# Kernel tuning notes

Hardware: AMD Instinct MI355X
Metric: run time of the kernel (lower is better)

## Reference

```python
import jax, jax.numpy as jnp
import numpy as np

N = 50000   # nodes
E = 800000  # edges
D = 64      # hidden_channels (= in_channels)
L = 3       # num_layers
G = 512     # graphs in batch
S = 32      # s_channels
BN_EPS = 1e-5


def setup_inputs() -> dict:
    key = jax.random.key(0)
    ks = jax.random.split(key, 10)
    x = jax.random.normal(ks[0], (N, D), dtype=jnp.float32)
    edge_index = jax.random.randint(ks[1], (2, E), 0, N)
    batch = jnp.sort(jax.random.randint(ks[2], (N,), 0, G))
    mapping = jax.random.randint(ks[3], (G,), 0, N)
    edge_weight = jax.random.uniform(ks[4], (E,), dtype=jnp.float32)
    pooling_mask = jnp.ones((N,), dtype=jnp.float32)
    # per-layer GIN MLP params (stacked over layers)
    W1 = 0.05 * jax.random.normal(ks[5], (L, D, D), dtype=jnp.float32)
    b1 = jnp.zeros((L, D), jnp.float32)
    gamma = jnp.ones((L, D), jnp.float32)
    beta = jnp.zeros((L, D), jnp.float32)
    bn_mean = jnp.zeros((L, D), jnp.float32)
    bn_var = jnp.ones((L, D), jnp.float32)
    W2 = 0.05 * jax.random.normal(ks[6], (L, D, D), dtype=jnp.float32)
    b2 = jnp.zeros((L, D), jnp.float32)
    eps = jnp.zeros((L,), jnp.float32)  # train_eps=True, init 0
    lin_w = 0.05 * jax.random.normal(ks[7], (2 * D * L, S), dtype=jnp.float32)
    lin_b = jnp.zeros((S,), jnp.float32)
    return dict(x=x, edge_weight=edge_weight, pooling_mask=pooling_mask,
                W1=W1, b1=b1, gamma=gamma, beta=beta, bn_mean=bn_mean,
                bn_var=bn_var, W2=W2, b2=b2, eps=eps, lin_w=lin_w,
                lin_b=lin_b, edge_index=edge_index, batch=batch,
                mapping=mapping)


def _sgin_forward(x, edge_weight, pooling_mask, W1, b1, gamma, beta,
                  bn_mean, bn_var, W2, b2, eps, lin_w, lin_b,
                  edge_index, batch, mapping):
    src, dst = edge_index[0], edge_index[1]
    h = x  # dropout is identity in eval mode
    pooled = []
    for i in range(L):
        # GIN aggregation: sum_j w_ij * h_j  at target nodes
        msg = h[src] * edge_weight[:, None]            # [E, D]
        agg = jax.ops.segment_sum(msg, dst, num_segments=N)
        z = (1.0 + eps[i]) * h + agg                   # [N, D]
        # MLP: Linear -> BN(eval) -> ReLU -> Linear -> ReLU
        z = z @ W1[i] + b1[i]
        z = gamma[i] * (z - bn_mean[i]) * jax.lax.rsqrt(bn_var[i] + BN_EPS) + beta[i]
        z = jax.nn.relu(z)
        h = jax.nn.relu(z @ W2[i] + b2[i])
        # per-layer pooling: masked global add pool || center-node gather
        emb_add = jax.ops.segment_sum(h * pooling_mask[:, None], batch,
                                      num_segments=G)  # [G, D]
        emb_center = h[mapping]                          # [G, D]
        pooled.append(jnp.concatenate([emb_add, emb_center], axis=-1))
    hcat = jnp.concatenate(pooled, axis=1)               # [G, 2*D*L]
    return hcat @ lin_w + lin_b                          # [G, S]


def reference(x, edge_weight, pooling_mask, W1, b1, gamma, beta, bn_mean,
              bn_var, W2, b2, eps, lin_w, lin_b, edge_index, batch, mapping):
    return _sgin_forward(x, edge_weight, pooling_mask, W1, b1, gamma, beta,
                         bn_mean, bn_var, W2, b2, eps, lin_w, lin_b,
                         edge_index, batch, mapping)
```

## Files before the change

### kernel.cpp

```cpp
#include <hip/hip_runtime.h>
#include <hip/hip_fp16.h>

#define DD 64
#define HC 384
#define SS 32
#define BINW 256
#define BSH 8
#define CAP 8192
#define CHUNK 4096

__global__ __launch_bounds__(256) void prep_kernel(
    const float* __restrict__ x, __half* __restrict__ hh0,
    int* __restrict__ bin_cur, float* __restrict__ hcat,
    int nbins, int hcat4, int total)
{
  int gid = blockIdx.x * 256 + threadIdx.x;
  if (gid < nbins) bin_cur[gid] = gid * CAP;
  if (gid < hcat4) ((float4*)hcat)[gid] = make_float4(0.f, 0.f, 0.f, 0.f);
  int i = gid * 8;
  if (i < total) {
    float4 a = *(const float4*)(x + i);
    float4 b = *(const float4*)(x + i + 4);
    __half2 o[4];
    o[0] = __floats2half2_rn(a.x, a.y);
    o[1] = __floats2half2_rn(a.z, a.w);
    o[2] = __floats2half2_rn(b.x, b.y);
    o[3] = __floats2half2_rn(b.z, b.w);
    *(float4*)(hh0 + i) = *(float4*)o;
  }
}

__global__ __launch_bounds__(256) void bin_part_kernel(
    const int* __restrict__ ei, const float* __restrict__ ew,
    int* __restrict__ bin_cur, unsigned* __restrict__ pk_slab,
    unsigned short* __restrict__ dl_slab, int E)
{
  __shared__ unsigned spk[CHUNK];
  __shared__ unsigned short sdst[CHUNK];
  __shared__ int bcnt[256], boff[256], bcur[256], gbase[256], stmp[256];
  int t = threadIdx.x;
  int e0 = blockIdx.x * CHUNK;
  int m = min(CHUNK, E - e0);
  bcnt[t] = 0;
  __syncthreads();
  for (int i = t; i < m; i += 256)
    atomicAdd(&bcnt[ei[E + e0 + i] >> BSH], 1);
  __syncthreads();
  int v = bcnt[t];
  stmp[t] = v;
  __syncthreads();
  for (int o = 1; o < 256; o <<= 1) {
    int u = (t >= o) ? stmp[t - o] : 0;
    __syncthreads();
    stmp[t] += u;
    __syncthreads();
  }
  boff[t] = stmp[t] - v;
  bcur[t] = stmp[t] - v;
  if (v > 0) gbase[t] = atomicAdd(&bin_cur[t], v);
  __syncthreads();
  for (int i = t; i < m; i += 256) {
    unsigned d = (unsigned)ei[E + e0 + i];
    int b = d >> BSH;
    int p = atomicAdd(&bcur[b], 1);
    unsigned short wh = __half_as_ushort(__float2half(ew[e0 + i]));
    spk[p] = (unsigned)ei[e0 + i] | ((unsigned)wh << 16);
    sdst[p] = (unsigned short)d;
  }
  __syncthreads();
  for (int i = t; i < m; i += 256) {
    unsigned short d = sdst[i];
    int b = d >> BSH;
    int g = gbase[b] + (i - boff[b]);
    pk_slab[g] = spk[i];
    dl_slab[g] = d;
  }
}

__global__ __launch_bounds__(256) void fine_csr_kernel(
    const unsigned* __restrict__ pk_slab,
    const unsigned short* __restrict__ dl_slab,
    const int* __restrict__ bin_cur, int* __restrict__ beg,
    int* __restrict__ endo, unsigned* __restrict__ packed, int N)
{
  __shared__ int cnt[256], loff[256], cur[256], stmp[256];
  int t = threadIdx.x;
  int b = blockIdx.x;
  int sbase = b * CAP;
  int m = bin_cur[b] - sbase;
  cnt[t] = 0;
  __syncthreads();
  for (int i = t; i < m; i += 256)
    atomicAdd(&cnt[dl_slab[sbase + i] & 255], 1);
  __syncthreads();
  int v = cnt[t];
  stmp[t] = v;
  __syncthreads();
  for (int o = 1; o < 256; o <<= 1) {
    int u = (t >= o) ? stmp[t - o] : 0;
    __syncthreads();
    stmp[t] += u;
    __syncthreads();
  }
  loff[t] = stmp[t] - v;
  cur[t] = loff[t];
  int node = b * BINW + t;
  if (node < N) {
    beg[node] = sbase + loff[t];
    endo[node] = sbase + loff[t] + v;
  }
  __syncthreads();
  for (int i = t; i < m; i += 256) {
    int dl = dl_slab[sbase + i] & 255;
    int p = atomicAdd(&cur[dl], 1);
    packed[sbase + p] = pk_slab[sbase + i];
  }
}

__global__ __launch_bounds__(256) void gather_kernel(
    const __half* __restrict__ hh, const unsigned* __restrict__ packed,
    const int* __restrict__ begA, const int* __restrict__ endA,
    const float* __restrict__ epsv, float* __restrict__ z, int layer, int N)
{
  int wave = threadIdx.x >> 6;
  int lane = threadIdx.x & 63;
  int sub = lane >> 3;
  int ch0 = (lane & 7) * 8;
  int na = blockIdx.x * 8 + wave * 2;
  int nb = na + 1;
  if (na >= N) return;
  bool hasB = nb < N;
  int bega = begA[na], enda = endA[na];
  int begb = hasB ? begA[nb] : 0, endb = hasB ? endA[nb] : 0;
  float accA[8] = {0, 0, 0, 0, 0, 0, 0, 0};
  float accB[8] = {0, 0, 0, 0, 0, 0, 0, 0};
  int ea = bega + sub, eb = begb + sub;
  while (ea < enda || eb < endb) {
    bool va = ea < enda;
    bool vb = eb < endb;
    unsigned pa = 0, pb = 0;
    if (va) pa = packed[ea];
    if (vb) pb = packed[eb];
    float4 ra, rb;
    if (va) ra = *(const float4*)(hh + (size_t)(pa & 0xffffu) * DD + ch0);
    if (vb) rb = *(const float4*)(hh + (size_t)(pb & 0xffffu) * DD + ch0);
    if (va) {
      float w = __half2float(__ushort_as_half((unsigned short)(pa >> 16)));
      const __half2* H = (const __half2*)&ra;
      #pragma unroll
      for (int j = 0; j < 4; ++j) {
        float2 f = __half22float2(H[j]);
        accA[2 * j]     = fmaf(w, f.x, accA[2 * j]);
        accA[2 * j + 1] = fmaf(w, f.y, accA[2 * j + 1]);
      }
    }
    if (vb) {
      float w = __half2float(__ushort_as_half((unsigned short)(pb >> 16)));
      const __half2* H = (const __half2*)&rb;
      #pragma unroll
      for (int j = 0; j < 4; ++j) {
        float2 f = __half22float2(H[j]);
        accB[2 * j]     = fmaf(w, f.x, accB[2 * j]);
        accB[2 * j + 1] = fmaf(w, f.y, accB[2 * j + 1]);
      }
    }
    ea += 8; eb += 8;
  }
  #pragma unroll
  for (int j = 0; j < 8; ++j) {
    accA[j] += __shfl_xor(accA[j], 8);
    accA[j] += __shfl_xor(accA[j], 16);
    accA[j] += __shfl_xor(accA[j], 32);
    accB[j] += __shfl_xor(accB[j], 8);
    accB[j] += __shfl_xor(accB[j], 16);
    accB[j] += __shfl_xor(accB[j], 32);
  }
  if (sub == 0) {
    float e1 = 1.0f + epsv[layer];
    {
      float4 sr = *(const float4*)(hh + (size_t)na * DD + ch0);
      const __half2* S = (const __half2*)&sr;
      float2 s0 = __half22float2(S[0]), s1 = __half22float2(S[1]);
      float2 s2 = __half22float2(S[2]), s3 = __half22float2(S[3]);
      float4 o0, o1;
      o0.x = fmaf(e1, s0.x, accA[0]); o0.y = fmaf(e1, s0.y, accA[1]);
      o0.z = fmaf(e1, s1.x, accA[2]); o0.w = fmaf(e1, s1.y, accA[3]);
      o1.x = fmaf(e1, s2.x, accA[4]); o1.y = fmaf(e1, s2.y, accA[5]);
      o1.z = fmaf(e1, s3.x, accA[6]); o1.w = fmaf(e1, s3.y, accA[7]);
      *(float4*)(z + (size_t)na * DD + ch0) = o0;
      *(float4*)(z + (size_t)na * DD + ch0 + 4) = o1;
    }
    if (hasB) {
      float4 sr = *(const float4*)(hh + (size_t)nb * DD + ch0);
      const __half2* S = (const __half2*)&sr;
      float2 s0 = __half22float2(S[0]), s1 = __half22float2(S[1]);
      float2 s2 = __half22float2(S[2]), s3 = __half22float2(S[3]);
      float4 o0, o1;
      o0.x = fmaf(e1, s0.x, accB[0]); o0.y = fmaf(e1, s0.y, accB[1]);
      o0.z = fmaf(e1, s1.x, accB[2]); o0.w = fmaf(e1, s1.y, accB[3]);
      o1.x = fmaf(e1, s2.x, accB[4]); o1.y = fmaf(e1, s2.y, accB[5]);
      o1.z = fmaf(e1, s3.x, accB[6]); o1.w = fmaf(e1, s3.y, accB[7]);
      *(float4*)(z + (size_t)nb * DD + ch0) = o0;
      *(float4*)(z + (size_t)nb * DD + ch0 + 4) = o1;
    }
  }
}

__global__ __launch_bounds__(256) void node_kernel(
    const float* __restrict__ z, __half* __restrict__ hhout,
    const float* __restrict__ W1, const float* __restrict__ b1,
    const float* __restrict__ gamma, const float* __restrict__ beta,
    const float* __restrict__ bnm, const float* __restrict__ bnv,
    const float* __restrict__ W2, const float* __restrict__ b2,
    const float* __restrict__ pmask, const int* __restrict__ batch,
    float* __restrict__ hcat, int layer, int N)
{
  __shared__ float tileZ[DD * DD];
  __shared__ float tileT[DD * DD];
  const int wave = threadIdx.x >> 6;
  const int lane = threadIdx.x & 63;
  const int n0 = blockIdx.x * 64;
  const int c0 = __builtin_amdgcn_readfirstlane(wave * 16);
  const float* W1l = W1 + layer * DD * DD;
  const float* W2l = W2 + layer * DD * DD;

  #pragma unroll
  for (int i = 0; i < 16; ++i) {
    int r = c0 + i;
    int n = n0 + r;
    float v = (n < N) ? z[(size_t)n * DD + lane] : 0.0f;
    tileZ[r * DD + ((lane + r) & 63)] = v;
  }
  __syncthreads();

  float t[16];
  #pragma unroll
  for (int cc = 0; cc < 16; ++cc) t[cc] = 0.0f;
  #pragma unroll 2
  for (int k = 0; k < DD; ++k) {
    float zk = tileZ[lane * DD + ((k + lane) & 63)];
    #pragma unroll
    for (int cc = 0; cc < 16; ++cc)
      t[cc] = fmaf(zk, W1l[k * DD + c0 + cc], t[cc]);
  }
  #pragma unroll
  for (int cc = 0; cc < 16; ++cc) {
    int c = c0 + cc;
    float A = gamma[layer * DD + c] * rsqrtf(bnv[layer * DD + c] + 1e-5f);
    float B = fmaf(b1[layer * DD + c] - bnm[layer * DD + c], A,
                   beta[layer * DD + c]);
    tileT[lane * DD + ((c + lane) & 63)] = fmaxf(fmaf(t[cc], A, B), 0.0f);
  }
  __syncthreads();

  #pragma unroll
  for (int cc = 0; cc < 16; ++cc) t[cc] = 0.0f;
  #pragma unroll 2
  for (int k = 0; k < DD; ++k) {
    float zk = tileT[lane * DD + ((k + lane) & 63)];
    #pragma unroll
    for (int cc = 0; cc < 16; ++cc)
      t[cc] = fmaf(zk, W2l[k * DD + c0 + cc], t[cc]);
  }
  #pragma unroll
  for (int cc = 0; cc < 16; ++cc) {
    int c = c0 + cc;
    tileZ[lane * DD + ((c + lane) & 63)] =
        fmaxf(t[cc] + b2[layer * DD + c], 0.0f);
  }
  __syncthreads();

  float accp = 0.0f;
  int gcur = -1;
  for (int i = 0; i < 16; ++i) {
    int r = c0 + i;
    int n = n0 + r;
    if (n >= N) break;
    float v = tileZ[r * DD + ((lane + r) & 63)];
    hhout[(size_t)n * DD + lane] = __float2half(v);
    int g = batch[n];
    if (g != gcur) {
      if (gcur >= 0) atomicAdd(&hcat[gcur * HC + layer * 128 + lane], accp);
      gcur = g; accp = 0.0f;
    }
    accp = fmaf(v, pmask[n], accp);
  }
  if (gcur >= 0) atomicAdd(&hcat[gcur * HC + layer * 128 + lane], accp);
}

__global__ __launch_bounds__(256) void final_kernel(
    const float* __restrict__ hcat, const __half* __restrict__ h1,
    const __half* __restrict__ h2, const __half* __restrict__ h3,
    const int* __restrict__ mapping, const float* __restrict__ lw,
    const float* __restrict__ lb, float* __restrict__ out, int G)
{
  int gid = blockIdx.x * 256 + threadIdx.x;
  int g = gid >> 5, s = gid & 31;
  if (g >= G) return;
  float acc = lb[s];
  size_t mrow = (size_t)mapping[g] * DD;
  #pragma unroll
  for (int l = 0; l < 3; ++l) {
    const float* hc = hcat + g * HC + l * 128;
    const float* lwa = lw + (l * 128) * SS + s;
    #pragma unroll 4
    for (int c = 0; c < 64; ++c)
      acc = fmaf(hc[c], lwa[c * SS], acc);
    const __half* hr = ((l == 0) ? h1 : ((l == 1) ? h2 : h3)) + mrow;
    const float* lwc = lw + (l * 128 + 64) * SS + s;
    #pragma unroll 4
    for (int c = 0; c < 64; ++c)
      acc = fmaf(__half2float(hr[c]), lwc[c * SS], acc);
  }
  out[g * SS + s] = acc;
}

extern "C" void kernel_launch(void* const* d_in, const int* in_sizes, int n_in,
                              void* d_out, int out_size, void* d_ws, size_t ws_size,
                              hipStream_t stream)
{
  const float* x     = (const float*)d_in[0];
  const float* ew    = (const float*)d_in[1];
  const float* pmask = (const float*)d_in[2];
  const float* W1    = (const float*)d_in[3];
  const float* b1    = (const float*)d_in[4];
  const float* gma   = (const float*)d_in[5];
  const float* bta   = (const float*)d_in[6];
  const float* bnm   = (const float*)d_in[7];
  const float* bnv   = (const float*)d_in[8];
  const float* W2    = (const float*)d_in[9];
  const float* b2    = (const float*)d_in[10];
  const float* epsv  = (const float*)d_in[11];
  const float* lw    = (const float*)d_in[12];
  const float* lb    = (const float*)d_in[13];
  const int*   ei    = (const int*)d_in[14];
  const int*   batch = (const int*)d_in[15];
  const int*   mapping = (const int*)d_in[16];

  const int N = in_sizes[2];
  const int E = in_sizes[1];
  const int G = in_sizes[16];
  const int nbins = (N + BINW - 1) / BINW;
  const int nchunks = (E + CHUNK - 1) / CHUNK;

  __half*   hh0  = (__half*)d_ws;
  __half*   hh1  = hh0 + (size_t)N * DD;
  __half*   hh2  = hh1 + (size_t)N * DD;
  __half*   hh3  = hh2 + (size_t)N * DD;
  float*    zscr = (float*)(hh3 + (size_t)N * DD);
  float*    hcat = zscr + (size_t)N * DD;
  int*      beg  = (int*)(hcat + (size_t)G * HC);
  int*      endo = beg + N;
  int*      bin_cur = endo + N;
  unsigned* packed  = (unsigned*)(bin_cur + 256);
  unsigned* pk_slab = packed + (size_t)nbins * CAP;
  unsigned short* dl_slab =
      (unsigned short*)(pk_slab + (size_t)nbins * CAP);
  float* fout = (float*)d_out;

  prep_kernel<<<(N * DD / 8 + 255) / 256, 256, 0, stream>>>(
      x, hh0, bin_cur, hcat, nbins, G * HC / 4, N * DD);

  bin_part_kernel<<<nchunks, 256, 0, stream>>>(ei, ew, bin_cur,
                                               pk_slab, dl_slab, E);
  fine_csr_kernel<<<nbins, 256, 0, stream>>>(pk_slab, dl_slab, bin_cur,
                                             beg, endo, packed, N);

  __half* hhs[4] = {hh0, hh1, hh2, hh3};
  for (int layer = 0; layer < 3; ++layer) {
    gather_kernel<<<(N + 7) / 8, 256, 0, stream>>>(
        hhs[layer], packed, beg, endo, epsv, zscr, layer, N);
    node_kernel<<<(N + 63) / 64, 256, 0, stream>>>(
        zscr, hhs[layer + 1], W1, b1, gma, bta, bnm, bnv, W2, b2,
        pmask, batch, hcat, layer, N);
  }
  final_kernel<<<(G * SS + 255) / 256, 256, 0, stream>>>(
      hcat, hh1, hh2, hh3, mapping, lw, lb, fout, G);
}
```

Measured before the change: 312.5 us.

## Run per-node GIN MLP on fp16 MFMA with prepacked weights and fp16 z

Replaces the scalar-FMA node MLP kernel with an MFMA 16x16x32 fp16 kernel. W1/W2 are repacked into the MFMA B-operand layout and the BN scale/shift is precomputed once in the prep kernel. The gather kernel now writes z in fp16 instead of fp32, which halves that intermediate's traffic. The edge partition chunk size is also halved. The cost is lower precision (fp16 z and weights) and an extra swizzled shared-memory staging step.

Measured after the change: 256.7 us. -17.9%, faster.

```diff
diff --git a/kernel.cpp b/kernel.cpp
--- a/kernel.cpp
+++ b/kernel.cpp
@@ -7,16 +7,47 @@
 #define BINW 256
 #define BSH 8
 #define CAP 8192
-#define CHUNK 4096
+#define CHUNK 2048
+
+typedef _Float16 f16x8v __attribute__((ext_vector_type(8)));
+typedef float f32x4v __attribute__((ext_vector_type(4)));
 
 __global__ __launch_bounds__(256) void prep_kernel(
     const float* __restrict__ x, __half* __restrict__ hh0,
     int* __restrict__ bin_cur, float* __restrict__ hcat,
-    int nbins, int hcat4, int total)
+    const float* __restrict__ W1, const float* __restrict__ W2,
+    const float* __restrict__ gma, const float* __restrict__ bta,
+    const float* __restrict__ bnm, const float* __restrict__ bnv,
+    const float* __restrict__ b1, __half* __restrict__ wpk,
+    float* __restrict__ abbn, int nbins, int hcat4, int total)
 {
   int gid = blockIdx.x * 256 + threadIdx.x;
   if (gid < nbins) bin_cur[gid] = gid * CAP;
   if (gid < hcat4) ((float4*)hcat)[gid] = make_float4(0.f, 0.f, 0.f, 0.f);
+  if (gid < 3072) {
+    int lane_ = gid & 63;
+    int rest = gid >> 6;
+    int kb = rest & 1;
+    int nt = (rest >> 1) & 3;
+    int gm = (rest >> 3) & 1;
+    int ly = rest >> 4;
+    const float* W = gm ? W2 : W1;
+    int c = nt * 16 + (lane_ & 15);
+    int k0 = kb * 32 + (lane_ >> 4) * 8;
+    f16x8v o;
+    #pragma unroll
+    for (int j = 0; j < 8; ++j)
+      o[j] = (_Float16)W[((size_t)ly * DD + k0 + j) * DD + c];
+    *(f16x8v*)(wpk + gid * 8) = o;
+  }
+  if (gid >= 4096 && gid < 4288) {
+    int id = gid - 4096;
+    int ly = id >> 6, c = id & 63;
+    float A = gma[ly * DD + c] * rsqrtf(bnv[ly * DD + c] + 1e-5f);
+    float B = fmaf(b1[ly * DD + c] - bnm[ly * DD + c], A, bta[ly * DD + c]);
+    abbn[ly * 128 + c] = A;
+    abbn[ly * 128 + 64 + c] = B;
+  }
   int i = gid * 8;
   if (i < total) {
     float4 a = *(const float4*)(x + i);
@@ -120,7 +151,7 @@
 __global__ __launch_bounds__(256) void gather_kernel(
     const __half* __restrict__ hh, const unsigned* __restrict__ packed,
     const int* __restrict__ begA, const int* __restrict__ endA,
-    const float* __restrict__ epsv, float* __restrict__ z, int layer, int N)
+    const float* __restrict__ epsv, __half* __restrict__ zh, int layer, int N)
 {
   int wave = threadIdx.x >> 6;
   int lane = threadIdx.x & 63;
@@ -180,108 +211,120 @@
     {
       float4 sr = *(const float4*)(hh + (size_t)na * DD + ch0);
       const __half2* S = (const __half2*)&sr;
-      float2 s0 = __half22float2(S[0]), s1 = __half22float2(S[1]);
-      float2 s2 = __half22float2(S[2]), s3 = __half22float2(S[3]);
-      float4 o0, o1;
-      o0.x = fmaf(e1, s0.x, accA[0]); o0.y = fmaf(e1, s0.y, accA[1]);
-      o0.z = fmaf(e1, s1.x, accA[2]); o0.w = fmaf(e1, s1.y, accA[3]);
-      o1.x = fmaf(e1, s2.x, accA[4]); o1.y = fmaf(e1, s2.y, accA[5]);
-      o1.z = fmaf(e1, s3.x, accA[6]); o1.w = fmaf(e1, s3.y, accA[7]);
-      *(float4*)(z + (size_t)na * DD + ch0) = o0;
-      *(float4*)(z + (size_t)na * DD + ch0 + 4) = o1;
+      f16x8v q;
+      #pragma unroll
+      for (int j = 0; j < 4; ++j) {
+        float2 f = __half22float2(S[j]);
+        q[2 * j]     = (_Float16)fmaf(e1, f.x, accA[2 * j]);
+        q[2 * j + 1] = (_Float16)fmaf(e1, f.y, accA[2 * j + 1]);
+      }
+      *(f16x8v*)(zh + (size_t)na * DD + ch0) = q;
     }
     if (hasB) {
       float4 sr = *(const float4*)(hh + (size_t)nb * DD + ch0);
       const __half2* S = (const __half2*)&sr;
-      float2 s0 = __half22float2(S[0]), s1 = __half22float2(S[1]);
-      float2 s2 = __half22float2(S[2]), s3 = __half22float2(S[3]);
-      float4 o0, o1;
-      o0.x = fmaf(e1, s0.x, accB[0]); o0.y = fmaf(e1, s0.y, accB[1]);
-      o0.z = fmaf(e1, s1.x, accB[2]); o0.w = fmaf(e1, s1.y, accB[3]);
-      o1.x = fmaf(e1, s2.x, accB[4]); o1.y = fmaf(e1, s2.y, accB[5]);
-      o1.z = fmaf(e1, s3.x, accB[6]); o1.w = fmaf(e1, s3.y, accB[7]);
-      *(float4*)(z + (size_t)nb * DD + ch0) = o0;
-      *(float4*)(z + (size_t)nb * DD + ch0 + 4) = o1;
-    }
-  }
-}
-
-__global__ __launch_bounds__(256) void node_kernel(
-    const float* __restrict__ z, __half* __restrict__ hhout,
-    const float* __restrict__ W1, const float* __restrict__ b1,
-    const float* __restrict__ gamma, const float* __restrict__ beta,
-    const float* __restrict__ bnm, const float* __restrict__ bnv,
-    const float* __restrict__ W2, const float* __restrict__ b2,
-    const float* __restrict__ pmask, const int* __restrict__ batch,
-    float* __restrict__ hcat, int layer, int N)
-{
-  __shared__ float tileZ[DD * DD];
-  __shared__ float tileT[DD * DD];
+      f16x8v q;
+      #pragma unroll
+      for (int j = 0; j < 4; ++j) {
+        float2 f = __half22float2(S[j]);
+        q[2 * j]     = (_Float16)fmaf(e1, f.x, accB[2 * j]);
+        q[2 * j + 1] = (_Float16)fmaf(e1, f.y, accB[2 * j + 1]);
+      }
+      *(f16x8v*)(zh + (size_t)nb * DD + ch0) = q;
+    }
+  }
+}
+
+__global__ __launch_bounds__(256) void node_mfma_kernel(
+    const __half* __restrict__ zh, __half* __restrict__ hhout,
+    const __half* __restrict__ wpk, const float* __restrict__ abbn,
+    const float* __restrict__ b2, const float* __restrict__ pmask,
+    const int* __restrict__ batch, float* __restrict__ hcat,
+    int layer, int N)
+{
+  __shared__ float tileF[DD * DD];
+  __half* tileH = (__half*)tileF;
   const int wave = threadIdx.x >> 6;
   const int lane = threadIdx.x & 63;
+  const int g = lane >> 4;
+  const int cr = lane & 15;
   const int n0 = blockIdx.x * 64;
-  const int c0 = __builtin_amdgcn_readfirstlane(wave * 16);
-  const float* W1l = W1 + layer * DD * DD;
-  const float* W2l = W2 + layer * DD * DD;
-
-  #pragma unroll
-  for (int i = 0; i < 16; ++i) {
-    int r = c0 + i;
-    int n = n0 + r;
-    float v = (n < N) ? z[(size_t)n * DD + lane] : 0.0f;
-    tileZ[r * DD + ((lane + r) & 63)] = v;
-  }
-  __syncthreads();
-
-  float t[16];
-  #pragma unroll
-  for (int cc = 0; cc < 16; ++cc) t[cc] = 0.0f;
-  #pragma unroll 2
-  for (int k = 0; k < DD; ++k) {
-    float zk = tileZ[lane * DD + ((k + lane) & 63)];
+  const int mrow = n0 + wave * 16 + cr;
+
+  const __half* wl  = wpk + (size_t)layer * 8192;
+  const __half* w2l = wl + 4096;
+
+  f16x8v a0 = *(const f16x8v*)(zh + (size_t)mrow * DD + g * 8);
+  f16x8v a1 = *(const f16x8v*)(zh + (size_t)mrow * DD + 32 + g * 8);
+  f32x4v acc[4];
+  #pragma unroll
+  for (int nt = 0; nt < 4; ++nt) {
+    f16x8v b0 = *(const f16x8v*)(wl + (nt * 2 + 0) * 512 + lane * 8);
+    f16x8v b1 = *(const f16x8v*)(wl + (nt * 2 + 1) * 512 + lane * 8);
+    acc[nt] = (f32x4v){0.f, 0.f, 0.f, 0.f};
+    acc[nt] = __builtin_amdgcn_mfma_f32_16x16x32_f16(a0, b0, acc[nt], 0, 0, 0);
+    acc[nt] = __builtin_amdgcn_mfma_f32_16x16x32_f16(a1, b1, acc[nt], 0, 0, 0);
+  }
+  #pragma unroll
+  for (int nt = 0; nt < 4; ++nt) {
+    int c = nt * 16 + cr;
+    float Ab = abbn[layer * 128 + c];
+    float Bb = abbn[layer * 128 + 64 + c];
     #pragma unroll
-    for (int cc = 0; cc < 16; ++cc)
-      t[cc] = fmaf(zk, W1l[k * DD + c0 + cc], t[cc]);
-  }
-  #pragma unroll
-  for (int cc = 0; cc < 16; ++cc) {
-    int c = c0 + cc;
-    float A = gamma[layer * DD + c] * rsqrtf(bnv[layer * DD + c] + 1e-5f);
-    float B = fmaf(b1[layer * DD + c] - bnm[layer * DD + c], A,
-                   beta[layer * DD + c]);
-    tileT[lane * DD + ((c + lane) & 63)] = fmaxf(fmaf(t[cc], A, B), 0.0f);
-  }
-  __syncthreads();
-
-  #pragma unroll
-  for (int cc = 0; cc < 16; ++cc) t[cc] = 0.0f;
-  #pragma unroll 2
-  for (int k = 0; k < DD; ++k) {
-    float zk = tileT[lane * DD + ((k + lane) & 63)];
+    for (int r = 0; r < 4; ++r) {
+      int row = wave * 16 + g * 4 + r;
+      float v = fmaxf(fmaf(acc[nt][r], Ab, Bb), 0.f);
+      tileH[row * DD + (((c >> 3) ^ (row & 7)) * 8) + (c & 7)] = __float2half(v);
+    }
+  }
+  __syncthreads();
+  const int arow = wave * 16 + cr;
+  f16x8v a20 = *(const f16x8v*)(tileH + arow * DD + ((g ^ (arow & 7)) * 8));
+  f16x8v a21 = *(const f16x8v*)(tileH + arow * DD + (((4 + g) ^ (arow & 7)) * 8));
+  f32x4v acc2[4];
+  #pragma unroll
+  for (int nt = 0; nt < 4; ++nt) {
+    f16x8v b0 = *(const f16x8v*)(w2l + (nt * 2 + 0) * 512 + lane * 8);
+    f16x8v b1 = *(const f16x8v*)(w2l + (nt * 2 + 1) * 512 + lane * 8);
+    acc2[nt] = (f32x4v){0.f, 0.f, 0.f, 0.f};
+    acc2[nt] = __builtin_amdgcn_mfma_f32_16x16x32_f16(a20, b0, acc2[nt], 0, 0, 0);
+    acc2[nt] = __builtin_amdgcn_mfma_f32_16x16x32_f16(a21, b1, acc2[nt], 0, 0, 0);
+  }
+  __syncthreads();
+  #pragma unroll
+  for (int nt = 0; nt < 4; ++nt) {
+    int c = nt * 16 + cr;
+    float bb = b2[layer * DD + c];
     #pragma unroll
-    for (int cc = 0; cc < 16; ++cc)
-      t[cc] = fmaf(zk, W2l[k * DD + c0 + cc], t[cc]);
-  }
-  #pragma unroll
-  for (int cc = 0; cc < 16; ++cc) {
-    int c = c0 + cc;
-    tileZ[lane * DD + ((c + lane) & 63)] =
-        fmaxf(t[cc] + b2[layer * DD + c], 0.0f);
-  }
-  __syncthreads();
-
+    for (int r = 0; r < 4; ++r) {
+      int row = wave * 16 + g * 4 + r;
+      tileF[row * DD + ((c + row) & 63)] = fmaxf(acc2[nt][r] + bb, 0.f);
+    }
+  }
+  __syncthreads();
+  #pragma unroll
+  for (int i = 0; i < 2; ++i) {
+    int id = i * 256 + threadIdx.x;
+    int rw = id >> 3, q = id & 7;
+    if (n0 + rw < N) {
+      f16x8v hv;
+      #pragma unroll
+      for (int j = 0; j < 8; ++j)
+        hv[j] = (_Float16)tileF[rw * DD + ((q * 8 + j + rw) & 63)];
+      *(f16x8v*)(hhout + (size_t)(n0 + rw) * DD + q * 8) = hv;
+    }
+  }
   float accp = 0.0f;
   int gcur = -1;
   for (int i = 0; i < 16; ++i) {
-    int r = c0 + i;
+    int r = wave * 16 + i;
     int n = n0 + r;
     if (n >= N) break;
-    float v = tileZ[r * DD + ((lane + r) & 63)];
-    hhout[(size_t)n * DD + lane] = __float2half(v);
-    int g = batch[n];
-    if (g != gcur) {
+    float v = tileF[r * DD + ((lane + r) & 63)];
+    int gb = batch[n];
+    if (gb != gcur) {
       if (gcur >= 0) atomicAdd(&hcat[gcur * HC + layer * 128 + lane], accp);
-      gcur = g; accp = 0.0f;
+      gcur = gb; accp = 0.0f;
     }
     accp = fmaf(v, pmask[n], accp);
   }
@@ -347,8 +390,9 @@
   __half*   hh1  = hh0 + (size_t)N * DD;
   __half*   hh2  = hh1 + (size_t)N * DD;
   __half*   hh3  = hh2 + (size_t)N * DD;
-  float*    zscr = (float*)(hh3 + (size_t)N * DD);
-  float*    hcat = zscr + (size_t)N * DD;
+  float*    zslab = (float*)(hh3 + (size_t)N * DD);
+  __half*   zh   = (__half*)zslab;
+  float*    hcat = zslab + (size_t)N * DD;
   int*      beg  = (int*)(hcat + (size_t)G * HC);
   int*      endo = beg + N;
   int*      bin_cur = endo + N;
@@ -356,10 +400,13 @@
   unsigned* pk_slab = packed + (size_t)nbins * CAP;
   unsigned short* dl_slab =
       (unsigned short*)(pk_slab + (size_t)nbins * CAP);
+  __half*   wpk  = (__half*)(dl_slab + (size_t)nbins * CAP);
+  float*    abbn = (float*)(wpk + 24576);
   float* fout = (float*)d_out;
 
   prep_kernel<<<(N * DD / 8 + 255) / 256, 256, 0, stream>>>(
-      x, hh0, bin_cur, hcat, nbins, G * HC / 4, N * DD);
+      x, hh0, bin_cur, hcat, W1, W2, gma, bta, bnm, bnv, b1,
+      wpk, abbn, nbins, G * HC / 4, N * DD);
 
   bin_part_kernel<<<nchunks, 256, 0, stream>>>(ei, ew, bin_cur,
                                                pk_slab, dl_slab, E);
@@ -369,10 +416,9 @@
   __half* hhs[4] = {hh0, hh1, hh2, hh3};
   for (int layer = 0; layer < 3; ++layer) {
     gather_kernel<<<(N + 7) / 8, 256, 0, stream>>>(
-        hhs[layer], packed, beg, endo, epsv, zscr, layer, N);
-    node_kernel<<<(N + 63) / 64, 256, 0, stream>>>(
-        zscr, hhs[layer + 1], W1, b1, gma, bta, bnm, bnv, W2, b2,
-        pmask, batch, hcat, layer, N);
+        hhs[layer], packed, beg, endo, epsv, zh, layer, N);
+    node_mfma_kernel<<<(N + 63) / 64, 256, 0, stream>>>(
+        zh, hhs[layer + 1], wpk, abbn, b2, pmask, batch, hcat, layer, N);
   }
   final_kernel<<<(G * SS + 255) / 256, 256, 0, stream>>>(
       hcat, hh1, hh2, hh3, mapping, lw, lb, fout, G);
```
